# Optimization experiments

Hardware: AMD Instinct MI355X
Metric: run time of the kernel (lower is better)

Reference implementation:

```python
import math
import jax, jax.numpy as jnp
import numpy as np

D_MODEL = 1024
N_HEAD = 16
HEAD_DIM = D_MODEL // N_HEAD
MAX_LENGTH = 2048


def sinusoid_table():
    # Matches RelativeEmbedding.get_embedding with num_embeddings = max_length + 1
    num_emb = MAX_LENGTH + 1
    half = HEAD_DIM // 2
    freq = jnp.exp(jnp.arange(half, dtype=jnp.float32) * (-math.log(10000.0) / (half - 1)))
    lo = -((num_emb + 1) // 2)  # python floor of -num_emb//2
    hi = num_emb // 2
    pos = jnp.arange(lo, hi, dtype=jnp.float32)  # length num_emb
    ang = pos[:, None] * freq[None, :]
    table = jnp.concatenate([jnp.sin(ang), jnp.cos(ang)], axis=1)  # (num_emb, HEAD_DIM)
    origin_shift = num_emb // 2 + 1
    return table, origin_shift


def _shift(BD):
    # (b, n, L, 2L) -> (b, n, L, L) diagonal-shift trick
    b, n, L, _ = BD.shape
    BD = jnp.concatenate([BD, jnp.zeros((b, n, L, 1), BD.dtype)], axis=-1)
    BD = BD.reshape(b, n, -1, L)[:, :, :-1, :].reshape(b, n, L, -1)
    return BD[:, :, :, :L]


def setup_inputs() -> dict:
    key = jax.random.key(0)
    k1, k2, k3, k4 = jax.random.split(key, 4)
    B, L = 2, 1024
    x = jax.random.normal(k1, (B, L, D_MODEL), dtype=jnp.float32)
    mask = jnp.ones((B, L), dtype=jnp.int32)
    W_qv = jax.random.normal(k2, (2 * D_MODEL, D_MODEL), dtype=jnp.float32) * 0.02
    r_r_bias = jax.random.normal(k3, (N_HEAD, HEAD_DIM), dtype=jnp.float32) * 0.02
    r_w_bias = jax.random.normal(k4, (N_HEAD, HEAD_DIM), dtype=jnp.float32) * 0.02
    return {"x": x, "mask": mask, "W_qv": W_qv, "r_r_bias": r_r_bias, "r_w_bias": r_w_bias}


def reference(x, mask, W_qv, r_r_bias, r_w_bias):
    B, L, d = x.shape
    table, origin_shift = sinusoid_table()
    pos = jnp.arange(-L, L) + origin_shift
    pos_embed = table[pos]  # (2L, head_dim)

    qv = x @ W_qv.T  # (B, L, 2d)
    q, v = jnp.split(qv, 2, axis=-1)
    q = q.reshape(B, L, N_HEAD, HEAD_DIM).transpose(0, 2, 1, 3)  # (B,H,L,dh)
    k = x.reshape(B, L, N_HEAD, HEAD_DIM).transpose(0, 2, 1, 3)
    v = v.reshape(B, L, N_HEAD, HEAD_DIM).transpose(0, 2, 1, 3)

    AC = jnp.einsum('bnqd,bnkd->bnqk', q + r_r_bias[None, :, None, :], k)
    D_ = jnp.einsum('nd,ld->nl', r_w_bias, pos_embed)[None, :, None, :]  # (1,H,1,2L)
    B_ = jnp.einsum('bnqd,ld->bnql', q, pos_embed)  # (B,H,L,2L)
    BD = _shift(B_ + D_)

    attn = AC + BD
    attn = jnp.where(mask[:, None, None, :] == 0, -jnp.inf, attn)
    attn = jax.nn.softmax(attn, axis=-1)
    out = jnp.einsum('bnqk,bnkd->bnqd', attn, v)
    return out.transpose(0, 2, 1, 3).reshape(B, L, d)
```

## Files before the change

### kernel.cpp

```cpp
#include <hip/hip_runtime.h>
#include <hip/hip_bf16.h>
#include <math.h>

#define L_SEQ 1024
#define TWO_L 2048
#define NHEAD 16
#define HD 64
#define DM 1024
#define BATCH 2
#define PE2R 2176
#define GBS 132

typedef _Float16 f16;
typedef _Float16 f16x4 __attribute__((ext_vector_type(4)));
typedef _Float16 f16x8 __attribute__((ext_vector_type(8)));
typedef float f32x4 __attribute__((ext_vector_type(4)));

__device__ __forceinline__ f16x8 ld8(const f16* p) {
  f16x4 lo = *(const f16x4*)p;
  f16x4 hi = *(const f16x4*)(p + 16);
  f16x8 r;
  r[0] = lo[0]; r[1] = lo[1]; r[2] = lo[2]; r[3] = lo[3];
  r[4] = hi[0]; r[5] = hi[1]; r[6] = hi[2]; r[7] = hi[3];
  return r;
}

__device__ __forceinline__ float pe_val(int j, int d) {
  float posval = (float)(j - L_SEQ);
  float freq = expf(-(float)(d & 31) * 0.2971077539347156f);
  float ang = posval * freq;
  return (d < 32) ? sinf(ang) : cosf(ang);
}

__global__ __launch_bounds__(256) void prep1(const float* __restrict__ x,
                                             const float* __restrict__ W,
                                             f16* __restrict__ pe2,
                                             f16* __restrict__ xh,
                                             f16* __restrict__ Wh) {
  int bid = blockIdx.x, tid = threadIdx.x;
  if (bid < 2048) {
    int i = (bid * 256 + tid) * 4;
    float4 v = *(const float4*)(x + i);
    f16x4 o = {(f16)v.x, (f16)v.y, (f16)v.z, (f16)v.w};
    *(f16x4*)(xh + i) = o;
  } else if (bid < 4096) {
    int i = ((bid - 2048) * 256 + tid) * 4;
    float4 v = *(const float4*)(W + i);
    f16x4 o = {(f16)v.x, (f16)v.y, (f16)v.z, (f16)v.w};
    *(f16x4*)(Wh + i) = o;
  } else {
    int idx = (bid - 4096) * 256 + tid;
    int rrow = idx >> 6, d = idx & 63;
    int u = rrow - 1088;
    int j = (u < 0) ? u + 2049 : u;
    float v = (j != 2048) ? pe_val(j, d) : 0.f;
    pe2[idx] = (f16)v;
  }
}

#define QV_STEP(T, AS, BS, CA0, CA1, CA2, CA3, CB0, CB1, NA0, NA1, NA2, NA3, NB0, NB1) \
  {                                                                            \
    *(f16x8*)&AS[ra * 72 + ca] = CA0;                                          \
    *(f16x8*)&AS[ra * 72 + ca + 8] = CA1;                                      \
    *(f16x8*)&AS[ra * 72 + ca + 16] = CA2;                                     \
    *(f16x8*)&AS[ra * 72 + ca + 24] = CA3;                                     \
    *(f16x8*)&BS[rb * 72 + cb] = CB0;                                          \
    *(f16x8*)&BS[rb * 72 + cb + 8] = CB1;                                      \
    __syncthreads();                                                           \
    if ((T) + 1 < 16) {                                                        \
      const f16* na = ga + ((T) + 1) * 64;                                     \
      NA0 = *(const f16x8*)na;                                                 \
      NA1 = *(const f16x8*)(na + 8);                                           \
      NA2 = *(const f16x8*)(na + 16);                                          \
      NA3 = *(const f16x8*)(na + 24);                                          \
      const f16* nb = gb + ((T) + 1) * 64;                                     \
      NB0 = *(const f16x8*)nb;                                                 \
      NB1 = *(const f16x8*)(nb + 8);                                           \
    }                                                                          \
    __builtin_amdgcn_s_setprio(1);                                             \
    _Pragma("unroll")                                                          \
    for (int kc = 0; kc < 2; ++kc) {                                           \
      f16x8 am0 = ld8(&AS[(w * 32 + li) * 72 + kc * 32 + g * 4]);              \
      f16x8 am1 = ld8(&AS[(w * 32 + 16 + li) * 72 + kc * 32 + g * 4]);         \
      _Pragma("unroll")                                                        \
      for (int nf = 0; nf < 4; ++nf) {                                         \
        f16x8 bfr = ld8(&BS[(nf * 16 + li) * 72 + kc * 32 + g * 4]);           \
        s[0][nf] = __builtin_amdgcn_mfma_f32_16x16x32_f16(am0, bfr, s[0][nf], 0, 0, 0); \
        s[1][nf] = __builtin_amdgcn_mfma_f32_16x16x32_f16(am1, bfr, s[1][nf], 0, 0, 0); \
      }                                                                        \
    }                                                                          \
    __builtin_amdgcn_s_setprio(0);                                             \
  }

__global__ __launch_bounds__(256) void qv_mfma(const f16* __restrict__ xh,
                                               const f16* __restrict__ Wh,
                                               f16* __restrict__ qvh,
                                               f16* __restrict__ vT) {
  __shared__ f16 As0[128 * 72], As1[128 * 72];
  __shared__ f16 Bs0[64 * 72], Bs1[64 * 72];
  int tid = threadIdx.x;
  int w = tid >> 6, lane = tid & 63, g = lane >> 4, li = lane & 15;
  int m0 = blockIdx.y * 128, n0 = blockIdx.x * 64;
  int ra = tid >> 1, ca = (tid & 1) * 32;
  int rb = tid >> 2, cb = (tid & 3) * 16;

  const f16* ga = xh + (size_t)(m0 + ra) * 1024 + ca;
  const f16* gb = Wh + (size_t)(n0 + rb) * 1024 + cb;
  f16x8 ca0 = *(const f16x8*)ga, ca1 = *(const f16x8*)(ga + 8);
  f16x8 ca2 = *(const f16x8*)(ga + 16), ca3 = *(const f16x8*)(ga + 24);
  f16x8 cb0 = *(const f16x8*)gb, cb1 = *(const f16x8*)(gb + 8);
  f16x8 na0, na1, na2, na3, nb0, nb1;

  f32x4 s[2][4];
#pragma unroll
  for (int i = 0; i < 2; ++i)
#pragma unroll
    for (int j = 0; j < 4; ++j) s[i][j] = {0.f, 0.f, 0.f, 0.f};

  for (int t = 0; t < 16; t += 2) {
    QV_STEP(t, As0, Bs0, ca0, ca1, ca2, ca3, cb0, cb1, na0, na1, na2, na3, nb0, nb1);
    QV_STEP(t + 1, As1, Bs1, na0, na1, na2, na3, nb0, nb1, ca0, ca1, ca2, ca3, cb0, cb1);
  }

#pragma unroll
  for (int mb = 0; mb < 2; ++mb) {
#pragma unroll
    for (int nf = 0; nf < 4; ++nf) {
      int n = n0 + nf * 16 + li;
#pragma unroll
      for (int rr2 = 0; rr2 < 4; ++rr2) {
        int m = m0 + w * 32 + mb * 16 + g * 4 + rr2;
        f16 val = (f16)s[mb][nf][rr2];
        if (n < 1024) {
          qvh[(size_t)m * 2048 + n] = val;
        } else {
          int b_ = m >> 10, ls = m & 1023, hd = n - 1024;
          vT[((size_t)(b_ * 16 + (hd >> 6)) * 64 + (hd & 63)) * 1024 + ls] = val;
        }
      }
    }
  }
}

#define BANDFILL(TT, QOFF, PEREG)                                              \
  {                                                                            \
    _Pragma("unroll")                                                          \
    for (int qf = 0; qf < 4; ++qf) {                                           \
      f32x4 gacc = {0.f, 0.f, 0.f, 0.f};                                       \
      _Pragma("unroll")                                                        \
      for (int kc = 0; kc < 2; ++kc) {                                         \
        f16x8 qo = ld8(&Qw[((QOFF) + qf * 16 + li) * 72 + kc * 32 + g * 4]);   \
        gacc = __builtin_amdgcn_mfma_f32_16x16x32_f16(PEREG[kc], qo, gacc, 0, 0, 0); \
      }                                                                        \
      f16x4 gpk;                                                               \
      gpk[0] = (f16)gacc[0]; gpk[1] = (f16)gacc[1];                            \
      gpk[2] = (f16)gacc[2]; gpk[3] = (f16)gacc[3];                            \
      *(f16x4*)&Gb[(qf * 16 + li) * GBS + (TT) + w * 16 + g * 4] = gpk;        \
    }                                                                          \
  }

#define ATTN_STEP(T, KS, VS, CK0, CK1, CV0, CV1, NK0, NK1, NV0, NV1, CPE, NPE) \
  {                                                                            \
    const int k0 = (T) * 64;                                                   \
    const int tt = (64 * (T)) & 127;                                           \
    const int qoff = (64 * (T) >= q0) ? 1 : 0;                                 \
    *(f16x8*)&KS[r * 72 + c] = CK0;                                            \
    *(f16x8*)&KS[r * 72 + c + 8] = CK1;                                        \
    *(f16x8*)&VS[r * 72 + c] = CV0;                                            \
    *(f16x8*)&VS[r * 72 + c + 8] = CV1;                                        \
    BANDFILL(tt, qoff, CPE)                                                    \
    __syncthreads();                                                           \
    if ((T) + 1 < 16) {                                                        \
      const f16* nk = gk + (size_t)((T) + 1) * 64 * 1024;                      \
      NK0 = *(const f16x8*)nk;                                                 \
      NK1 = *(const f16x8*)(nk + 8);                                           \
      const f16* nv = gv + ((T) + 1) * 64;                                     \
      NV0 = *(const f16x8*)nv;                                                 \
      NV1 = *(const f16x8*)(nv + 8);                                           \
      const f16* pb = pe2 + (size_t)(1088 + 64 * ((T) + 1) - q0 + w * 16 + li) * 64; \
      NPE[0] = ld8(pb + g * 4);                                                \
      NPE[1] = ld8(pb + 32 + g * 4);                                           \
    }                                                                          \
    float gf[16];                                                              \
    {                                                                          \
      const int cb0 = tt + g * 4 - qi + 128;                                   \
      _Pragma("unroll")                                                        \
      for (int kf = 0; kf < 4; ++kf)                                           \
        _Pragma("unroll")                                                      \
        for (int u2 = 0; u2 < 4; ++u2)                                         \
          gf[kf * 4 + u2] = (float)Gb[qi * GBS + ((cb0 + kf * 16 + u2) & 127)];\
    }                                                                          \
    f32x4 s[4];                                                                \
    _Pragma("unroll")                                                          \
    for (int i = 0; i < 4; ++i) s[i] = {0.f, 0.f, 0.f, 0.f};                   \
    __builtin_amdgcn_s_setprio(1);                                             \
    _Pragma("unroll")                                                          \
    for (int kc = 0; kc < 2; ++kc) {                                           \
      f16x8 qb = ld8(&Qs[(1 + w * 16 + li) * 72 + kc * 32 + g * 4]);           \
      _Pragma("unroll")                                                        \
      for (int kf = 0; kf < 4; ++kf) {                                         \
        f16x8 ka = ld8(&KS[(kf * 16 + li) * 72 + kc * 32 + g * 4]);            \
        s[kf] = __builtin_amdgcn_mfma_f32_16x16x32_f16(ka, qb, s[kf], 0, 0, 0);\
      }                                                                        \
    }                                                                          \
    __builtin_amdgcn_s_setprio(0);                                             \
    float sv[16];                                                              \
    float tmax = -1e30f;                                                       \
    _Pragma("unroll")                                                          \
    for (int kf = 0; kf < 4; ++kf) {                                           \
      _Pragma("unroll")                                                        \
      for (int rr2 = 0; rr2 < 4; ++rr2) {                                      \
        float v_ = s[kf][rr2] + gf[kf * 4 + rr2] +                             \
                   Ms[k0 + kf * 16 + g * 4 + rr2];                             \
        sv[kf * 4 + rr2] = v_;                                                 \
        tmax = fmaxf(tmax, v_);                                                \
      }                                                                        \
    }                                                                          \
    tmax = fmaxf(tmax, __shfl_xor(tmax, 16));                                  \
    tmax = fmaxf(tmax, __shfl_xor(tmax, 32));                                  \
    if (!__all(tmax <= m_run + 8.f)) {                                         \
      float mnew = fmaxf(m_run, tmax);                                         \
      float scale = __expf(m_run - mnew);                                      \
      m_run = mnew;                                                            \
      l_run *= scale;                                                          \
      _Pragma("unroll")                                                        \
      for (int f = 0; f < 4; ++f) {                                            \
        o[f][0] *= scale; o[f][1] *= scale; o[f][2] *= scale; o[f][3] *= scale;\
      }                                                                        \
    }                                                                          \
    float pf[16];                                                              \
    float lloc = 0.f;                                                          \
    _Pragma("unroll")                                                          \
    for (int i = 0; i < 16; ++i) { pf[i] = __expf(sv[i] - m_run); lloc += pf[i]; } \
    l_run += lloc;                                                             \
    f16x8 pb0, pb1;                                                            \
    _Pragma("unroll")                                                          \
    for (int i = 0; i < 8; ++i) { pb0[i] = (f16)pf[i]; pb1[i] = (f16)pf[8 + i]; } \
    __builtin_amdgcn_s_setprio(1);                                             \
    _Pragma("unroll")                                                          \
    for (int f = 0; f < 4; ++f) {                                              \
      f16x8 va0 = ld8(&VS[(f * 16 + li) * 72 + g * 4]);                        \
      o[f] = __builtin_amdgcn_mfma_f32_16x16x32_f16(va0, pb0, o[f], 0, 0, 0);  \
      f16x8 va1 = ld8(&VS[(f * 16 + li) * 72 + 32 + g * 4]);                   \
      o[f] = __builtin_amdgcn_mfma_f32_16x16x32_f16(va1, pb1, o[f], 0, 0, 0);  \
    }                                                                          \
    __builtin_amdgcn_s_setprio(0);                                             \
    __syncthreads();                                                           \
  }

__global__ __launch_bounds__(256) void attn_mfma(const f16* __restrict__ xh,
                                                 const f16* __restrict__ qvh,
                                                 const f16* __restrict__ vT,
                                                 const f16* __restrict__ pe2,
                                                 const int* __restrict__ mask,
                                                 const float* __restrict__ rr,
                                                 const float* __restrict__ rw,
                                                 float* __restrict__ out) {
  __shared__ f16 Qs[65 * 72];
  __shared__ f16 Qw[65 * 72];
  __shared__ f16 Ks0[64 * 72], Ks1[64 * 72];
  __shared__ f16 Vs0[64 * 72], Vs1[64 * 72];
  __shared__ f16 Gb[64 * GBS];
  __shared__ float Ms[L_SEQ];
  int tid = threadIdx.x;
  int w = tid >> 6, lane = tid & 63, g = lane >> 4, li = lane & 15;
  int bid = blockIdx.x;
  int swz = (bid & 7) * 64 + (bid >> 3);
  int q0 = (swz & 15) * 64;
  int bh = swz >> 4;
  int b = bh >> 4, h = bh & 15;
  int r = tid >> 2, c = (tid & 3) * 16;
  const int qi = w * 16 + li;

#pragma unroll
  for (int i = 0; i < 4; ++i) {
    int k = tid + i * 256;
    Ms[k] = mask[b * L_SEQ + k] ? 0.f : -1e30f;
  }
  {
    int gq = q0 - 1 + r;
    if (gq < 0) gq = 0;
    const f16* src = qvh + (size_t)(b * L_SEQ + gq) * 2048 + h * HD + c;
#pragma unroll
    for (int u = 0; u < 16; ++u) {
      float v = (float)src[u];
      Qs[r * 72 + c + u] = (f16)(v + rr[h * HD + c + u]);
      Qw[r * 72 + c + u] = (f16)(v + rw[h * HD + c + u]);
    }
    if (tid < 4) {
      int c2 = tid * 16;
      const f16* s2 = qvh + (size_t)(b * L_SEQ + q0 + 63) * 2048 + h * HD + c2;
#pragma unroll
      for (int u = 0; u < 16; ++u) {
        float v = (float)s2[u];
        Qs[64 * 72 + c2 + u] = (f16)(v + rr[h * HD + c2 + u]);
        Qw[64 * 72 + c2 + u] = (f16)(v + rw[h * HD + c2 + u]);
      }
    }
  }

  const f16* gk = xh + (size_t)(b * L_SEQ + r) * 1024 + h * HD + c;
  const f16* gv = vT + ((size_t)bh * 64 + r) * 1024 + c;
  f16x8 cka = *(const f16x8*)gk, ckb = *(const f16x8*)(gk + 8);
  f16x8 cva = *(const f16x8*)gv, cvb = *(const f16x8*)(gv + 8);
  f16x8 nka, nkb, nva, nvb;
  f16x8 peP[2], peA[2], peB[2];
  {
    const f16* pp = pe2 + (size_t)(1024 - q0 + w * 16 + li) * 64;
    peP[0] = ld8(pp + g * 4);
    peP[1] = ld8(pp + 32 + g * 4);
    const f16* p0 = pe2 + (size_t)(1088 - q0 + w * 16 + li) * 64;
    peA[0] = ld8(p0 + g * 4);
    peA[1] = ld8(p0 + 32 + g * 4);
  }

  __syncthreads();

  BANDFILL(64, 0, peP)

  float m_run = -1e30f, l_run = 0.f;
  f32x4 o[4];
#pragma unroll
  for (int i = 0; i < 4; ++i) o[i] = {0.f, 0.f, 0.f, 0.f};

  for (int t = 0; t < 16; t += 2) {
    ATTN_STEP(t, Ks0, Vs0, cka, ckb, cva, cvb, nka, nkb, nva, nvb, peA, peB);
    ATTN_STEP(t + 1, Ks1, Vs1, nka, nkb, nva, nvb, cka, ckb, cva, cvb, peB, peA);
  }

  float lt = l_run;
  lt += __shfl_xor(lt, 16);
  lt += __shfl_xor(lt, 32);
  float inv = 1.0f / lt;
  int qrow = q0 + qi;
  float* op = out + ((size_t)(b * L_SEQ + qrow)) * DM + h * HD;
#pragma unroll
  for (int f = 0; f < 4; ++f) {
    float4 res = {o[f][0] * inv, o[f][1] * inv, o[f][2] * inv, o[f][3] * inv};
    *(float4*)(op + f * 16 + g * 4) = res;
  }
}

extern "C" void kernel_launch(void* const* d_in, const int* in_sizes, int n_in,
                              void* d_out, int out_size, void* d_ws, size_t ws_size,
                              hipStream_t stream) {
  const float* x = (const float*)d_in[0];
  const int* mask = (const int*)d_in[1];
  const float* W = (const float*)d_in[2];
  const float* rr = (const float*)d_in[3];
  const float* rw = (const float*)d_in[4];
  float* out = (float*)d_out;

  f16* pe2 = (f16*)d_ws;
  f16* xh = pe2 + (size_t)PE2R * 64;
  f16* Wh = xh + 2097152;
  f16* qvh = Wh + 2097152;
  f16* vT = qvh + 4194304;

  prep1<<<4096 + (PE2R * 64) / 256, 256, 0, stream>>>(x, W, pe2, xh, Wh);
  qv_mfma<<<dim3(32, 16), 256, 0, stream>>>(xh, Wh, qvh, vT);
  attn_mfma<<<512, 256, 0, stream>>>(xh, qvh, vT, pe2, mask, rr, rw, out);
}
```

Baseline: 79.65 us.

## Precompute positional bias term and pipeline band fill one tile ahead

The r_w_bias positional term is rewritten as q+r_r times pe plus a precomputed per-head (rw-rr)·pe vector. Extra blocks in the QV GEMM kernel compute that vector, which removes the second biased Q copy (Qw) from shared memory. The band-fill MFMA for the next key tile now runs before the barrier, using a triple-buffered Gb, and K/V staging is reorganised so each step writes the next tile while reading the current one. This shortens the critical path per step and cuts LDS use, but adds a small extra kernel workload and changes fp16 rounding of the bias term.

```diff
diff --git a/kernel.cpp b/kernel.cpp
--- a/kernel.cpp
+++ b/kernel.cpp
@@ -9,7 +9,6 @@
 #define DM 1024
 #define BATCH 2
 #define PE2R 2176
-#define GBS 132
 
 typedef _Float16 f16;
 typedef _Float16 f16x4 __attribute__((ext_vector_type(4)));
@@ -95,12 +94,29 @@
 __global__ __launch_bounds__(256) void qv_mfma(const f16* __restrict__ xh,
                                                const f16* __restrict__ Wh,
                                                f16* __restrict__ qvh,
-                                               f16* __restrict__ vT) {
+                                               f16* __restrict__ vT,
+                                               const float* __restrict__ rr,
+                                               const float* __restrict__ rw,
+                                               const f16* __restrict__ pe2,
+                                               float* __restrict__ D2x) {
   __shared__ f16 As0[128 * 72], As1[128 * 72];
   __shared__ f16 Bs0[64 * 72], Bs1[64 * 72];
   int tid = threadIdx.x;
+  int bid = blockIdx.x;
+  if (bid >= 512) {
+    int idx = (bid - 512) * 256 + tid;
+    if (idx < 16 * PE2R) {
+      int h = idx / PE2R, r0 = idx - h * PE2R;
+      float s = 0.f;
+#pragma unroll
+      for (int d = 0; d < HD; ++d)
+        s = fmaf(rw[h * HD + d] - rr[h * HD + d], (float)pe2[r0 * HD + d], s);
+      D2x[idx] = s;
+    }
+    return;
+  }
   int w = tid >> 6, lane = tid & 63, g = lane >> 4, li = lane & 15;
-  int m0 = blockIdx.y * 128, n0 = blockIdx.x * 64;
+  int m0 = (bid >> 5) * 128, n0 = (bid & 31) * 64;
   int ra = tid >> 1, ca = (tid & 1) * 32;
   int rb = tid >> 2, cb = (tid & 3) * 16;
 
@@ -142,53 +158,59 @@
   }
 }
 
-#define BANDFILL(TT, QOFF, PEREG)                                              \
+#define BANDFILL(GW, QOFF, PEREG, D2V)                                         \
   {                                                                            \
     _Pragma("unroll")                                                          \
     for (int qf = 0; qf < 4; ++qf) {                                           \
       f32x4 gacc = {0.f, 0.f, 0.f, 0.f};                                       \
       _Pragma("unroll")                                                        \
       for (int kc = 0; kc < 2; ++kc) {                                         \
-        f16x8 qo = ld8(&Qw[((QOFF) + qf * 16 + li) * 72 + kc * 32 + g * 4]);   \
+        f16x8 qo = ld8(&Qs[((QOFF) + qf * 16 + li) * 72 + kc * 32 + g * 4]);   \
         gacc = __builtin_amdgcn_mfma_f32_16x16x32_f16(PEREG[kc], qo, gacc, 0, 0, 0); \
       }                                                                        \
       f16x4 gpk;                                                               \
-      gpk[0] = (f16)gacc[0]; gpk[1] = (f16)gacc[1];                            \
-      gpk[2] = (f16)gacc[2]; gpk[3] = (f16)gacc[3];                            \
-      *(f16x4*)&Gb[(qf * 16 + li) * GBS + (TT) + w * 16 + g * 4] = gpk;        \
-    }                                                                          \
-  }
-
-#define ATTN_STEP(T, KS, VS, CK0, CK1, CV0, CV1, NK0, NK1, NV0, NV1, CPE, NPE) \
+      gpk[0] = (f16)(gacc[0] + (D2V).x); gpk[1] = (f16)(gacc[1] + (D2V).y);    \
+      gpk[2] = (f16)(gacc[2] + (D2V).z); gpk[3] = (f16)(gacc[3] + (D2V).w);    \
+      *(f16x4*)&(GW)[(qf * 16 + li) * 68 + w * 16 + g * 4] = gpk;              \
+    }                                                                          \
+  }
+
+#define ATTN_STEP(T, KSW, VSW, KSR, VSR, CK0, CK1, CV0, CV1, NK0, NK1, NV0, NV1, CPE, NPE) \
   {                                                                            \
     const int k0 = (T) * 64;                                                   \
-    const int tt = (64 * (T)) & 127;                                           \
-    const int qoff = (64 * (T) >= q0) ? 1 : 0;                                 \
-    *(f16x8*)&KS[r * 72 + c] = CK0;                                            \
-    *(f16x8*)&KS[r * 72 + c + 8] = CK1;                                        \
-    *(f16x8*)&VS[r * 72 + c] = CV0;                                            \
-    *(f16x8*)&VS[r * 72 + c + 8] = CV1;                                        \
-    BANDFILL(tt, qoff, CPE)                                                    \
-    __syncthreads();                                                           \
     if ((T) + 1 < 16) {                                                        \
-      const f16* nk = gk + (size_t)((T) + 1) * 64 * 1024;                      \
+      *(f16x8*)&KSW[r * 72 + c] = CK0;                                         \
+      *(f16x8*)&KSW[r * 72 + c + 8] = CK1;                                     \
+      *(f16x8*)&VSW[r * 72 + c] = CV0;                                         \
+      *(f16x8*)&VSW[r * 72 + c + 8] = CV1;                                     \
+      const int qoff = (64 * ((T) + 1) >= q0) ? 1 : 0;                         \
+      float4 d2v = *(const float4*)(D2x + hD2 + 1088 + 64 * ((T) + 1) - q0 + w * 16 + g * 4); \
+      BANDFILL(gpN, qoff, CPE, d2v)                                            \
+    }                                                                          \
+    if ((T) + 2 < 16) {                                                        \
+      const f16* nk = gk + (size_t)((T) + 2) * 64 * 1024;                      \
       NK0 = *(const f16x8*)nk;                                                 \
       NK1 = *(const f16x8*)(nk + 8);                                           \
-      const f16* nv = gv + ((T) + 1) * 64;                                     \
+      const f16* nv = gv + ((T) + 2) * 64;                                     \
       NV0 = *(const f16x8*)nv;                                                 \
       NV1 = *(const f16x8*)(nv + 8);                                           \
-      const f16* pb = pe2 + (size_t)(1088 + 64 * ((T) + 1) - q0 + w * 16 + li) * 64; \
+      const f16* pb = pe2 + (size_t)(1088 + 64 * ((T) + 2) - q0 + w * 16 + li) * 64; \
       NPE[0] = ld8(pb + g * 4);                                                \
       NPE[1] = ld8(pb + 32 + g * 4);                                           \
     }                                                                          \
     float gf[16];                                                              \
     {                                                                          \
-      const int cb0 = tt + g * 4 - qi + 128;                                   \
-      _Pragma("unroll")                                                        \
-      for (int kf = 0; kf < 4; ++kf)                                           \
+      const f16* baseT = gpT + qi * 68 - qi;                                   \
+      const f16* baseP = gpP + qi * 68 - qi + 64;                              \
+      _Pragma("unroll")                                                        \
+      for (int kf = 0; kf < 4; ++kf) {                                         \
         _Pragma("unroll")                                                      \
-        for (int u2 = 0; u2 < 4; ++u2)                                         \
-          gf[kf * 4 + u2] = (float)Gb[qi * GBS + ((cb0 + kf * 16 + u2) & 127)];\
+        for (int u2 = 0; u2 < 4; ++u2) {                                       \
+          const int koff = kf * 16 + g * 4 + u2;                               \
+          const f16* p = (koff >= qi ? baseT : baseP) + koff;                  \
+          gf[kf * 4 + u2] = (float)*p;                                         \
+        }                                                                      \
+      }                                                                        \
     }                                                                          \
     f32x4 s[4];                                                                \
     _Pragma("unroll")                                                          \
@@ -199,7 +221,7 @@
       f16x8 qb = ld8(&Qs[(1 + w * 16 + li) * 72 + kc * 32 + g * 4]);           \
       _Pragma("unroll")                                                        \
       for (int kf = 0; kf < 4; ++kf) {                                         \
-        f16x8 ka = ld8(&KS[(kf * 16 + li) * 72 + kc * 32 + g * 4]);            \
+        f16x8 ka = ld8(&KSR[(kf * 16 + li) * 72 + kc * 32 + g * 4]);           \
         s[kf] = __builtin_amdgcn_mfma_f32_16x16x32_f16(ka, qb, s[kf], 0, 0, 0);\
       }                                                                        \
     }                                                                          \
@@ -239,28 +261,28 @@
     __builtin_amdgcn_s_setprio(1);                                             \
     _Pragma("unroll")                                                          \
     for (int f = 0; f < 4; ++f) {                                              \
-      f16x8 va0 = ld8(&VS[(f * 16 + li) * 72 + g * 4]);                        \
+      f16x8 va0 = ld8(&VSR[(f * 16 + li) * 72 + g * 4]);                       \
       o[f] = __builtin_amdgcn_mfma_f32_16x16x32_f16(va0, pb0, o[f], 0, 0, 0);  \
-      f16x8 va1 = ld8(&VS[(f * 16 + li) * 72 + 32 + g * 4]);                   \
+      f16x8 va1 = ld8(&VSR[(f * 16 + li) * 72 + 32 + g * 4]);                  \
       o[f] = __builtin_amdgcn_mfma_f32_16x16x32_f16(va1, pb1, o[f], 0, 0, 0);  \
     }                                                                          \
     __builtin_amdgcn_s_setprio(0);                                             \
     __syncthreads();                                                           \
+    { f16* tmpg = gpP; gpP = gpT; gpT = gpN; gpN = tmpg; }                     \
   }
 
 __global__ __launch_bounds__(256) void attn_mfma(const f16* __restrict__ xh,
                                                  const f16* __restrict__ qvh,
                                                  const f16* __restrict__ vT,
                                                  const f16* __restrict__ pe2,
+                                                 const float* __restrict__ D2x,
                                                  const int* __restrict__ mask,
                                                  const float* __restrict__ rr,
-                                                 const float* __restrict__ rw,
                                                  float* __restrict__ out) {
   __shared__ f16 Qs[65 * 72];
-  __shared__ f16 Qw[65 * 72];
   __shared__ f16 Ks0[64 * 72], Ks1[64 * 72];
   __shared__ f16 Vs0[64 * 72], Vs1[64 * 72];
-  __shared__ f16 Gb[64 * GBS];
+  __shared__ f16 Gb0[64 * 68], Gb1[64 * 68], Gb2[64 * 68];
   __shared__ float Ms[L_SEQ];
   int tid = threadIdx.x;
   int w = tid >> 6, lane = tid & 63, g = lane >> 4, li = lane & 15;
@@ -271,6 +293,7 @@
   int b = bh >> 4, h = bh & 15;
   int r = tid >> 2, c = (tid & 3) * 16;
   const int qi = w * 16 + li;
+  const int hD2 = h * PE2R;
 
 #pragma unroll
   for (int i = 0; i < 4; ++i) {
@@ -282,41 +305,65 @@
     if (gq < 0) gq = 0;
     const f16* src = qvh + (size_t)(b * L_SEQ + gq) * 2048 + h * HD + c;
 #pragma unroll
-    for (int u = 0; u < 16; ++u) {
-      float v = (float)src[u];
-      Qs[r * 72 + c + u] = (f16)(v + rr[h * HD + c + u]);
-      Qw[r * 72 + c + u] = (f16)(v + rw[h * HD + c + u]);
-    }
+    for (int u = 0; u < 16; ++u)
+      Qs[r * 72 + c + u] = (f16)((float)src[u] + rr[h * HD + c + u]);
     if (tid < 4) {
       int c2 = tid * 16;
       const f16* s2 = qvh + (size_t)(b * L_SEQ + q0 + 63) * 2048 + h * HD + c2;
 #pragma unroll
-      for (int u = 0; u < 16; ++u) {
-        float v = (float)s2[u];
-        Qs[64 * 72 + c2 + u] = (f16)(v + rr[h * HD + c2 + u]);
-        Qw[64 * 72 + c2 + u] = (f16)(v + rw[h * HD + c2 + u]);
-      }
+      for (int u = 0; u < 16; ++u)
+        Qs[64 * 72 + c2 + u] = (f16)((float)s2[u] + rr[h * HD + c2 + u]);
     }
   }
 
   const f16* gk = xh + (size_t)(b * L_SEQ + r) * 1024 + h * HD + c;
   const f16* gv = vT + ((size_t)bh * 64 + r) * 1024 + c;
-  f16x8 cka = *(const f16x8*)gk, ckb = *(const f16x8*)(gk + 8);
-  f16x8 cva = *(const f16x8*)gv, cvb = *(const f16x8*)(gv + 8);
-  f16x8 nka, nkb, nva, nvb;
-  f16x8 peP[2], peA[2], peB[2];
+  {
+    f16x8 t0k0 = *(const f16x8*)gk, t0k1 = *(const f16x8*)(gk + 8);
+    f16x8 t0v0 = *(const f16x8*)gv, t0v1 = *(const f16x8*)(gv + 8);
+    *(f16x8*)&Ks0[r * 72 + c] = t0k0;
+    *(f16x8*)&Ks0[r * 72 + c + 8] = t0k1;
+    *(f16x8*)&Vs0[r * 72 + c] = t0v0;
+    *(f16x8*)&Vs0[r * 72 + c + 8] = t0v1;
+  }
+  f16x8 pePm1[2], pe0[2];
   {
     const f16* pp = pe2 + (size_t)(1024 - q0 + w * 16 + li) * 64;
-    peP[0] = ld8(pp + g * 4);
-    peP[1] = ld8(pp + 32 + g * 4);
+    pePm1[0] = ld8(pp + g * 4);
+    pePm1[1] = ld8(pp + 32 + g * 4);
     const f16* p0 = pe2 + (size_t)(1088 - q0 + w * 16 + li) * 64;
-    peA[0] = ld8(p0 + g * 4);
-    peA[1] = ld8(p0 + 32 + g * 4);
+    pe0[0] = ld8(p0 + g * 4);
+    pe0[1] = ld8(p0 + 32 + g * 4);
   }
 
   __syncthreads();
 
-  BANDFILL(64, 0, peP)
+  {
+    float4 d2m1 = *(const float4*)(D2x + hD2 + 1024 - q0 + w * 16 + g * 4);
+    BANDFILL(Gb2, 0, pePm1, d2m1)
+    const int qoff0 = (q0 == 0) ? 1 : 0;
+    float4 d20 = *(const float4*)(D2x + hD2 + 1088 - q0 + w * 16 + g * 4);
+    BANDFILL(Gb0, qoff0, pe0, d20)
+  }
+  f16x8 cka, ckb, cva, cvb, nka, nkb, nva, nvb;
+  f16x8 peA[2], peB[2];
+  {
+    const f16* nk = gk + (size_t)64 * 1024;
+    cka = *(const f16x8*)nk;
+    ckb = *(const f16x8*)(nk + 8);
+    const f16* nv = gv + 64;
+    cva = *(const f16x8*)nv;
+    cvb = *(const f16x8*)(nv + 8);
+    const f16* pb = pe2 + (size_t)(1088 + 64 - q0 + w * 16 + li) * 64;
+    peA[0] = ld8(pb + g * 4);
+    peA[1] = ld8(pb + 32 + g * 4);
+  }
+
+  __syncthreads();
+
+  f16* gpP = Gb2;
+  f16* gpT = Gb0;
+  f16* gpN = Gb1;
 
   float m_run = -1e30f, l_run = 0.f;
   f32x4 o[4];
@@ -324,8 +371,8 @@
   for (int i = 0; i < 4; ++i) o[i] = {0.f, 0.f, 0.f, 0.f};
 
   for (int t = 0; t < 16; t += 2) {
-    ATTN_STEP(t, Ks0, Vs0, cka, ckb, cva, cvb, nka, nkb, nva, nvb, peA, peB);
-    ATTN_STEP(t + 1, Ks1, Vs1, nka, nkb, nva, nvb, cka, ckb, cva, cvb, peB, peA);
+    ATTN_STEP(t, Ks1, Vs1, Ks0, Vs0, cka, ckb, cva, cvb, nka, nkb, nva, nvb, peA, peB);
+    ATTN_STEP(t + 1, Ks0, Vs0, Ks1, Vs1, nka, nkb, nva, nvb, cka, ckb, cva, cvb, peB, peA);
   }
 
   float lt = l_run;
@@ -352,12 +399,13 @@
   float* out = (float*)d_out;
 
   f16* pe2 = (f16*)d_ws;
-  f16* xh = pe2 + (size_t)PE2R * 64;
+  float* D2x = (float*)(pe2 + (size_t)PE2R * 64);
+  f16* xh = (f16*)(D2x + 16 * PE2R);
   f16* Wh = xh + 2097152;
   f16* qvh = Wh + 2097152;
   f16* vT = qvh + 4194304;
 
   prep1<<<4096 + (PE2R * 64) / 256, 256, 0, stream>>>(x, W, pe2, xh, Wh);
-  qv_mfma<<<dim3(32, 16), 256, 0, stream>>>(xh, Wh, qvh, vT);
-  attn_mfma<<<512, 256, 0, stream>>>(xh, qvh, vT, pe2, mask, rr, rw, out);
-}
+  qv_mfma<<<512 + (16 * PE2R + 255) / 256, 256, 0, stream>>>(xh, Wh, qvh, vT, rr, rw, pe2, D2x);
+  attn_mfma<<<512, 256, 0, stream>>>(xh, qvh, vT, pe2, D2x, mask, rr, out);
+}
```

Result: slower. 84.35 us (+5.9%).
